# Kernel optimization log

Measured on AMD Instinct MI355X. Metric: run time of the kernel, lower is better.

The kernel has to match this reference:

```python
import math
import jax, jax.numpy as jnp
import numpy as np

L = 2          # num_layers
B = 2          # micro batch
S = 2048       # seq_length
H = 1024       # hidden_size
NH = 16        # num_attention_heads
DH = 64        # kv_channels (head dim)
FF = 4096      # ffn_hidden_size
EPS = 1e-5
STD = 0.0048


def setup_inputs() -> dict:
    key = jax.random.key(0)
    ks = jax.random.split(key, 12)
    out_std = STD / math.sqrt(2.0 * L)
    # ALiBi slopes for NH=16 (power of 2)
    start = 2.0 ** (-2.0 ** (-(math.log2(NH) - 3)))
    slopes = np.array([start * start ** i for i in range(NH)], dtype=np.float32)
    alibi = slopes[None, :, None, None] * np.arange(S, dtype=np.float32)[None, None, None, :]
    alibi = jnp.asarray(np.broadcast_to(alibi, (B, NH, 1, S)))  # [B, NH, 1, S]
    return {
        "hidden_states": jax.random.normal(ks[0], (B, S, H), jnp.float32),
        "alibi": alibi,
        "qkv_w": jax.random.normal(ks[1], (L, 3 * NH * DH, H), jnp.float32) * STD,
        "qkv_b": jnp.zeros((L, 3 * NH * DH), jnp.float32),
        "dense_w": jax.random.normal(ks[2], (L, H, NH * DH), jnp.float32) * out_std,
        "dense_b": jnp.zeros((L, H), jnp.float32),
        "mlp_w1": jax.random.normal(ks[3], (L, FF, H), jnp.float32) * STD,
        "mlp_b1": jnp.zeros((L, FF), jnp.float32),
        "mlp_w2": jax.random.normal(ks[4], (L, H, FF), jnp.float32) * out_std,
        "mlp_b2": jnp.zeros((L, H), jnp.float32),
        "ln1_w": jnp.ones((L, H), jnp.float32),
        "ln1_b": jnp.zeros((L, H), jnp.float32),
        "ln2_w": jnp.ones((L, H), jnp.float32),
        "ln2_b": jnp.zeros((L, H), jnp.float32),
    }


def _layernorm(x, w, b):
    mu = jnp.mean(x, axis=-1, keepdims=True)
    var = jnp.mean(jnp.square(x - mu), axis=-1, keepdims=True)
    return (x - mu) * jax.lax.rsqrt(var + EPS) * w + b


def _layer(x, alibi, causal, layer_number, qkv_w, qkv_b, dense_w, dense_b,
           mlp_w1, mlp_b1, mlp_w2, mlp_b2, ln1_w, ln1_b, ln2_w, ln2_b):
    # --- attention ---
    h = _layernorm(x, ln1_w, ln1_b)
    qkv = h @ qkv_w.T + qkv_b                       # [B, S, 3*NH*DH]
    q, k, v = jnp.split(qkv, 3, axis=-1)
    q = q.reshape(B, S, NH, DH).transpose(0, 2, 1, 3)  # [B, NH, S, DH]
    k = k.reshape(B, S, NH, DH).transpose(0, 2, 1, 3)
    v = v.reshape(B, S, NH, DH).transpose(0, 2, 1, 3)
    norm_factor = math.sqrt(DH) * layer_number
    beta = 1.0 / layer_number
    alpha = 1.0 / norm_factor
    scores = beta * alibi + alpha * jnp.einsum("bhqd,bhkd->bhqk", q, k)
    # ScaleMaskSoftmax: scale by layer_number, causal mask fill -10000, softmax
    scores = scores * layer_number
    scores = jnp.where(causal, scores, jnp.float32(-10000.0))
    probs = jax.nn.softmax(scores, axis=-1)
    ctx = jnp.einsum("bhqk,bhkd->bhqd", probs, v)   # [B, NH, S, DH]
    ctx = ctx.transpose(0, 2, 1, 3).reshape(B, S, NH * DH)
    attn_out = ctx @ dense_w.T + dense_b
    x = x + attn_out
    # --- MLP ---
    h2 = _layernorm(x, ln2_w, ln2_b)
    m = jax.nn.gelu(h2 @ mlp_w1.T + mlp_b1, approximate=False)
    m = m @ mlp_w2.T + mlp_b2
    return x + m


def reference(hidden_states, alibi, qkv_w, qkv_b, dense_w, dense_b,
              mlp_w1, mlp_b1, mlp_w2, mlp_b2, ln1_w, ln1_b, ln2_w, ln2_b):
    causal = jnp.tril(jnp.ones((S, S), dtype=bool))[None, None]  # [1,1,S,S]
    x = hidden_states
    for l in range(L):
        x = _layer(x, alibi, causal, l + 1,
                   qkv_w[l], qkv_b[l], dense_w[l], dense_b[l],
                   mlp_w1[l], mlp_b1[l], mlp_w2[l], mlp_b2[l],
                   ln1_w[l], ln1_b[l], ln2_w[l], ln2_b[l])
    return x
```

## Files before the change

### kernel.cpp

```cpp
#include <hip/hip_runtime.h>
#include <cstdint>
#include <cmath>

#define SS 2048
#define HH 1024

typedef __bf16 bf16_t;
typedef __bf16 bf16x8 __attribute__((ext_vector_type(8)));
typedef __bf16 bf16x4 __attribute__((ext_vector_type(4)));
typedef float  f32x4  __attribute__((ext_vector_type(4)));

union U32P { unsigned u; bf16_t h[2]; };

__device__ __forceinline__ void async_load16(const void* g, void* l) {
  __builtin_amdgcn_global_load_lds(
      (__attribute__((address_space(1))) void*)(g),
      (__attribute__((address_space(3))) void*)(l), 16, 0, 0);
}

__device__ __forceinline__ void bar_lds() {
  asm volatile("s_waitcnt lgkmcnt(0)" ::: "memory");
  __builtin_amdgcn_s_barrier();
}

__global__ __launch_bounds__(256) void cvt_kernel(const float* __restrict__ in,
                                                  bf16_t* __restrict__ out) {
  size_t i = (size_t)blockIdx.x * 256 + threadIdx.x;
  f32x4 v = ((const f32x4*)in)[i];
  bf16x4 o;
  o[0] = (bf16_t)v[0]; o[1] = (bf16_t)v[1]; o[2] = (bf16_t)v[2]; o[3] = (bf16_t)v[3];
  ((bf16x4*)out)[i] = o;
}

__global__ __launch_bounds__(256) void ln_kernel(const float* __restrict__ x,
                                                 const float* __restrict__ w,
                                                 const float* __restrict__ b,
                                                 bf16_t* __restrict__ out) {
  const int row = blockIdx.x;
  const int tid = threadIdx.x;
  const f32x4 v = ((const f32x4*)(x + (size_t)row * HH))[tid];
  float s  = v[0] + v[1] + v[2] + v[3];
  float s2 = v[0]*v[0] + v[1]*v[1] + v[2]*v[2] + v[3]*v[3];
#pragma unroll
  for (int o = 1; o < 64; o <<= 1) { s += __shfl_xor(s, o); s2 += __shfl_xor(s2, o); }
  __shared__ float r1[4], r2[4];
  if ((tid & 63) == 0) { r1[tid >> 6] = s; r2[tid >> 6] = s2; }
  __syncthreads();
  float ts  = r1[0] + r1[1] + r1[2] + r1[3];
  float ts2 = r2[0] + r2[1] + r2[2] + r2[3];
  float mu  = ts * (1.0f / HH);
  float var = ts2 * (1.0f / HH) - mu * mu;
  float rstd = rsqrtf(var + 1e-5f);
  f32x4 wv = ((const f32x4*)w)[tid];
  f32x4 bv = ((const f32x4*)b)[tid];
  bf16x4 o;
#pragma unroll
  for (int j = 0; j < 4; ++j) o[j] = (bf16_t)((v[j] - mu) * rstd * wv[j] + bv[j]);
  ((bf16x4*)(out + (size_t)row * HH))[tid] = o;
}

__device__ __forceinline__ float gelu_f(float x) {
  return 0.5f * x * (1.0f + erff(x * 0.70710678118654752f));
}

__global__ __launch_bounds__(256) void fuse_add(float* __restrict__ x,
                                                const bf16_t* __restrict__ p0,
                                                const bf16_t* __restrict__ p1,
                                                const float* __restrict__ bias) {
  size_t i = (size_t)blockIdx.x * 256 + threadIdx.x;
  f32x4 xv = ((f32x4*)x)[i];
  bf16x4 a = ((const bf16x4*)p0)[i];
  bf16x4 b4 = ((const bf16x4*)p1)[i];
  f32x4 bv = ((const f32x4*)bias)[i & 255];
#pragma unroll
  for (int j = 0; j < 4; ++j) xv[j] += (float)a[j] + (float)b4[j] + bv[j];
  ((f32x4*)x)[i] = xv;
}

template <int EPI>
__global__ __launch_bounds__(256) void gemm_bt(const bf16_t* __restrict__ A,
                                               const bf16_t* __restrict__ W,
                                               const float* __restrict__ bias,
                                               bf16_t* __restrict__ outb,
                                               int M, int N, int K) {
  __shared__ __align__(16) bf16_t As[128 * 64];
  __shared__ __align__(16) bf16_t Bs[128 * 64];
  const int tid = threadIdx.x;
  const int w = tid >> 6, lane = tid & 63;
  const int m16 = lane & 15, quad = lane >> 4;
  const int wm = w & 1, wn = w >> 1;
  const int n0 = blockIdx.x * 128, m0 = blockIdx.y * 128;

  f32x4 acc[4][4];
#pragma unroll
  for (int i = 0; i < 4; ++i)
#pragma unroll
    for (int j = 0; j < 4; ++j) acc[i][j] = (f32x4){0.f, 0.f, 0.f, 0.f};

  int rowi[4], gci[4];
#pragma unroll
  for (int i = 0; i < 4; ++i) {
    int p = (w * 4 + i) * 64 + lane;
    rowi[i] = p >> 3;
    gci[i] = ((lane & 7) ^ (rowi[i] & 7)) * 8;
  }

  for (int kt = 0; kt < K; kt += 64) {
    __syncthreads();
#pragma unroll
    for (int i = 0; i < 4; ++i) {
      async_load16(A + (size_t)(m0 + rowi[i]) * K + kt + gci[i], &As[(w * 4 + i) * 512]);
      async_load16(W + (size_t)(n0 + rowi[i]) * K + kt + gci[i], &Bs[(w * 4 + i) * 512]);
    }
    __syncthreads();
#pragma unroll
    for (int kk = 0; kk < 2; ++kk) {
      bf16x8 af[4], bfv[4];
#pragma unroll
      for (int mi = 0; mi < 4; ++mi) {
        int row = wm * 64 + mi * 16 + m16;
        int cpos = (kk * 4 + quad) ^ (row & 7);
        af[mi] = *(const bf16x8*)&As[row * 64 + cpos * 8];
      }
#pragma unroll
      for (int ni = 0; ni < 4; ++ni) {
        int row = wn * 64 + ni * 16 + m16;
        int cpos = (kk * 4 + quad) ^ (row & 7);
        bfv[ni] = *(const bf16x8*)&Bs[row * 64 + cpos * 8];
      }
#pragma unroll
      for (int mi = 0; mi < 4; ++mi)
#pragma unroll
        for (int ni = 0; ni < 4; ++ni)
          acc[mi][ni] = __builtin_amdgcn_mfma_f32_16x16x32_bf16(af[mi], bfv[ni],
                                                                acc[mi][ni], 0, 0, 0);
    }
  }

#pragma unroll
  for (int ni = 0; ni < 4; ++ni) {
    int col = n0 + wn * 64 + ni * 16 + m16;
    float bv = bias[col];
#pragma unroll
    for (int mi = 0; mi < 4; ++mi) {
      int rowb = m0 + wm * 64 + mi * 16 + quad * 4;
#pragma unroll
      for (int r = 0; r < 4; ++r) {
        size_t idx = (size_t)(rowb + r) * N + col;
        float v = acc[mi][ni][r] + bv;
        if constexpr (EPI == 1) v = gelu_f(v);
        outb[idx] = (bf16_t)v;
      }
    }
  }
}

__global__ __launch_bounds__(256) void gemm_qkv(const bf16_t* __restrict__ A,
                                                const bf16_t* __restrict__ W,
                                                const float* __restrict__ bias,
                                                bf16_t* __restrict__ qc,
                                                bf16_t* __restrict__ kc,
                                                bf16_t* __restrict__ vc) {
  const int M = 4096, N = 3072, K = 1024;
  __shared__ __align__(16) bf16_t As[128 * 64];
  __shared__ __align__(16) bf16_t Bs[128 * 64];
  const int tid = threadIdx.x;
  const int w = tid >> 6, lane = tid & 63;
  const int m16 = lane & 15, quad = lane >> 4;
  const int wm = w & 1, wn = w >> 1;
  const int n0 = blockIdx.x * 128, m0 = blockIdx.y * 128;

  f32x4 acc[4][4];
#pragma unroll
  for (int i = 0; i < 4; ++i)
#pragma unroll
    for (int j = 0; j < 4; ++j) acc[i][j] = (f32x4){0.f, 0.f, 0.f, 0.f};

  int rowi[4], gci[4];
#pragma unroll
  for (int i = 0; i < 4; ++i) {
    int p = (w * 4 + i) * 64 + lane;
    rowi[i] = p >> 3;
    gci[i] = ((lane & 7) ^ (rowi[i] & 7)) * 8;
  }

  for (int kt = 0; kt < K; kt += 64) {
    __syncthreads();
#pragma unroll
    for (int i = 0; i < 4; ++i) {
      async_load16(A + (size_t)(m0 + rowi[i]) * K + kt + gci[i], &As[(w * 4 + i) * 512]);
      async_load16(W + (size_t)(n0 + rowi[i]) * K + kt + gci[i], &Bs[(w * 4 + i) * 512]);
    }
    __syncthreads();
#pragma unroll
    for (int kk = 0; kk < 2; ++kk) {
      bf16x8 af[4], bfv[4];
#pragma unroll
      for (int mi = 0; mi < 4; ++mi) {
        int row = wm * 64 + mi * 16 + m16;
        int cpos = (kk * 4 + quad) ^ (row & 7);
        af[mi] = *(const bf16x8*)&As[row * 64 + cpos * 8];
      }
#pragma unroll
      for (int ni = 0; ni < 4; ++ni) {
        int row = wn * 64 + ni * 16 + m16;
        int cpos = (kk * 4 + quad) ^ (row & 7);
        bfv[ni] = *(const bf16x8*)&Bs[row * 64 + cpos * 8];
      }
#pragma unroll
      for (int mi = 0; mi < 4; ++mi)
#pragma unroll
        for (int ni = 0; ni < 4; ++ni)
          acc[mi][ni] = __builtin_amdgcn_mfma_f32_16x16x32_bf16(af[mi], bfv[ni],
                                                                acc[mi][ni], 0, 0, 0);
    }
  }

  const int bb = m0 >> 11;
  const int sbase = (m0 & 2047) + wm * 64;
#pragma unroll
  for (int ni = 0; ni < 4; ++ni) {
    int col = n0 + wn * 64 + ni * 16 + m16;
    float bv = bias[col];
    int region = col >> 10;
    int h = (col >> 6) & 15, d = col & 63;
#pragma unroll
    for (int mi = 0; mi < 4; ++mi) {
#pragma unroll
      for (int r = 0; r < 4; ++r) {
        int s = sbase + mi * 16 + quad * 4 + r;
        float v = acc[mi][ni][r] + bv;
        if (region == 0) {
          qc[(size_t)(bb * SS + s) * 1024 + col] = (bf16_t)v;
        } else {
          bf16_t* o = (region == 1) ? kc : vc;
          o[((size_t)(bb * 16 + h) * SS + s) * 64 + d] = (bf16_t)v;
        }
      }
    }
  }
}

__global__ __launch_bounds__(256) void gemm_sk2(const bf16_t* __restrict__ A,
                                                const bf16_t* __restrict__ W,
                                                bf16_t* __restrict__ p0,
                                                bf16_t* __restrict__ p1,
                                                int M, int N, int K) {
  __shared__ __align__(16) bf16_t As[128 * 64];
  __shared__ __align__(16) bf16_t Bs[128 * 64];
  const int tid = threadIdx.x;
  const int w = tid >> 6, lane = tid & 63;
  const int m16 = lane & 15, quad = lane >> 4;
  const int wm = w & 1, wn = w >> 1;
  const int n0 = blockIdx.x * 128, m0 = blockIdx.y * 128;
  const int z = blockIdx.z;
  const int kbeg = z * (K >> 1), kend = kbeg + (K >> 1);
  bf16_t* outb = z ? p1 : p0;

  f32x4 acc[4][4];
#pragma unroll
  for (int i = 0; i < 4; ++i)
#pragma unroll
    for (int j = 0; j < 4; ++j) acc[i][j] = (f32x4){0.f, 0.f, 0.f, 0.f};

  int rowi[4], gci[4];
#pragma unroll
  for (int i = 0; i < 4; ++i) {
    int p = (w * 4 + i) * 64 + lane;
    rowi[i] = p >> 3;
    gci[i] = ((lane & 7) ^ (rowi[i] & 7)) * 8;
  }

  for (int kt = kbeg; kt < kend; kt += 64) {
    __syncthreads();
#pragma unroll
    for (int i = 0; i < 4; ++i) {
      async_load16(A + (size_t)(m0 + rowi[i]) * K + kt + gci[i], &As[(w * 4 + i) * 512]);
      async_load16(W + (size_t)(n0 + rowi[i]) * K + kt + gci[i], &Bs[(w * 4 + i) * 512]);
    }
    __syncthreads();
#pragma unroll
    for (int kk = 0; kk < 2; ++kk) {
      bf16x8 af[4], bfv[4];
#pragma unroll
      for (int mi = 0; mi < 4; ++mi) {
        int row = wm * 64 + mi * 16 + m16;
        int cpos = (kk * 4 + quad) ^ (row & 7);
        af[mi] = *(const bf16x8*)&As[row * 64 + cpos * 8];
      }
#pragma unroll
      for (int ni = 0; ni < 4; ++ni) {
        int row = wn * 64 + ni * 16 + m16;
        int cpos = (kk * 4 + quad) ^ (row & 7);
        bfv[ni] = *(const bf16x8*)&Bs[row * 64 + cpos * 8];
      }
#pragma unroll
      for (int mi = 0; mi < 4; ++mi)
#pragma unroll
        for (int ni = 0; ni < 4; ++ni)
          acc[mi][ni] = __builtin_amdgcn_mfma_f32_16x16x32_bf16(af[mi], bfv[ni],
                                                                acc[mi][ni], 0, 0, 0);
    }
  }

#pragma unroll
  for (int ni = 0; ni < 4; ++ni) {
    int col = n0 + wn * 64 + ni * 16 + m16;
#pragma unroll
    for (int mi = 0; mi < 4; ++mi) {
      int rowb = m0 + wm * 64 + mi * 16 + quad * 4;
#pragma unroll
      for (int r = 0; r < 4; ++r) {
        size_t idx = (size_t)(rowb + r) * N + col;
        outb[idx] = (bf16_t)acc[mi][ni][r];
      }
    }
  }
}

__global__ __launch_bounds__(256) void attn_kernel(const bf16_t* __restrict__ qc,
                                                   const bf16_t* __restrict__ kc,
                                                   const bf16_t* __restrict__ vcp,
                                                   bf16_t* __restrict__ ctx,
                                                   bf16_t* __restrict__ pa0,
                                                   float* __restrict__ pl0,
                                                   bf16_t* __restrict__ pa1,
                                                   float* __restrict__ pl1) {
  const int qt = 31 - blockIdx.y;
  const int bh = blockIdx.x;
  const int b = bh >> 4, h = bh & 15;
  const int tid = threadIdx.x;
  const int w = tid >> 6, lane = tid & 63;
  const int m16 = lane & 15, quad = lane >> 4;

  const float slope2 = __builtin_amdgcn_exp2f(-0.70710678118654752f * (float)(h + 1))
                       * 1.4426950408889634f;
  const int wt = (int)((30.0f / slope2 + 63.0f) * 0.015625f);
  const int kt0 = (qt - wt > 0) ? (qt - wt) : 0;
  const int nch = (qt - kt0 + 8) >> 3;
  const int z = blockIdx.z;
  if (z >= nch) return;
  const int ktb = kt0 + z * 8;
  const int kte = (ktb + 7 < qt) ? (ktb + 7) : qt;
  const bool multi = (nch > 1);

  __shared__ __align__(16) bf16_t Vt[2][64 * 72];
  __shared__ __align__(16) bf16_t Pl[4][16 * 72];

  const int q_abs = qt * 64 + w * 16 + m16;
  float alkb[16];
#pragma unroll
  for (int kn = 0; kn < 4; ++kn)
#pragma unroll
    for (int r = 0; r < 4; ++r)
      alkb[kn * 4 + r] = slope2 * (float)(ktb * 64 + kn * 16 + quad * 4 + r - q_abs);
  const float d64 = slope2 * 64.0f;

  const int qrow = qt * 64 + w * 16 + m16;
  const bf16_t* qbase = qc + (size_t)(b * SS + qrow) * 1024 + h * 64;
  const bf16x8 bq0 = *(const bf16x8*)(qbase + quad * 8);
  const bf16x8 bq1 = *(const bf16x8*)(qbase + 32 + quad * 8);

  const bf16_t* kbase = kc + ((size_t)(b * 16 + h) * SS + m16) * 64 + quad * 8;
  const int kp2 = (tid & 31) * 2, vd0 = (tid >> 5) * 8;
  const bf16_t* vsrc = vcp + ((size_t)(b * 16 + h) * SS + kp2) * 64 + vd0;
  const int ql = w * 16 + m16;
  constexpr float C = 0.18033688011112042f;

  f32x4 acc[4];
#pragma unroll
  for (int i = 0; i < 4; ++i) acc[i] = (f32x4){0.f, 0.f, 0.f, 0.f};
  float rs_l = 0.f;

  bf16x8 ak[4][2], v0, v1;
  {
    const bf16_t* kb = kbase + (size_t)ktb * 4096;
#pragma unroll
    for (int kn = 0; kn < 4; ++kn) {
      ak[kn][0] = *(const bf16x8*)(kb + kn * 1024);
      ak[kn][1] = *(const bf16x8*)(kb + kn * 1024 + 32);
    }
    const bf16_t* vs = vsrc + (size_t)ktb * 4096;
    v0 = *(const bf16x8*)(vs);
    v1 = *(const bf16x8*)(vs + 64);
  }
#pragma unroll
  for (int j = 0; j < 8; ++j) {
    U32P pk; pk.h[0] = v0[j]; pk.h[1] = v1[j];
    *(unsigned*)&Vt[ktb & 1][(vd0 + j) * 72 + kp2] = pk.u;
  }

  for (int kt = ktb; kt <= kte; ++kt) {
    bar_lds();

    bf16x8 nk[4][2], nv0 = v0, nv1 = v1;
    if (kt < kte) {
      const bf16_t* kb = kbase + (size_t)(kt + 1) * 4096;
#pragma unroll
      for (int kn = 0; kn < 4; ++kn) {
        nk[kn][0] = *(const bf16x8*)(kb + kn * 1024);
        nk[kn][1] = *(const bf16x8*)(kb + kn * 1024 + 32);
      }
      const bf16_t* nsrc = vsrc + (size_t)(kt + 1) * 4096;
      nv0 = *(const bf16x8*)(nsrc);
      nv1 = *(const bf16x8*)(nsrc + 64);
    } else {
#pragma unroll
      for (int kn = 0; kn < 4; ++kn) { nk[kn][0] = ak[kn][0]; nk[kn][1] = ak[kn][1]; }
    }

    __builtin_amdgcn_s_setprio(1);
    float p[16];
    const bool diag = (kt == qt);
#pragma unroll
    for (int kn = 0; kn < 4; ++kn) {
      f32x4 zz = (f32x4){0.f, 0.f, 0.f, 0.f};
      zz = __builtin_amdgcn_mfma_f32_16x16x32_bf16(ak[kn][0], bq0, zz, 0, 0, 0);
      zz = __builtin_amdgcn_mfma_f32_16x16x32_bf16(ak[kn][1], bq1, zz, 0, 0, 0);
#pragma unroll
      for (int r = 0; r < 4; ++r) {
        float s = fmaf(zz[r], C, alkb[kn * 4 + r]);
        if (diag) {
          int kl = kn * 16 + quad * 4 + r;
          if (kl > ql) s = -INFINITY;
        }
        float e = __builtin_amdgcn_exp2f(s);
        p[kn * 4 + r] = e;
        rs_l += e;
      }
    }
#pragma unroll
    for (int i = 0; i < 16; ++i) alkb[i] += d64;

#pragma unroll
    for (int kn = 0; kn < 4; ++kn) {
      U32P a, c;
      a.h[0] = (bf16_t)p[kn * 4 + 0]; a.h[1] = (bf16_t)p[kn * 4 + 1];
      c.h[0] = (bf16_t)p[kn * 4 + 2]; c.h[1] = (bf16_t)p[kn * 4 + 3];
      uint2 pk; pk.x = a.u; pk.y = c.u;
      *(uint2*)&Pl[w][m16 * 72 + kn * 16 + quad * 4] = pk;
    }
    const bf16_t* vt = &Vt[kt & 1][0];
    bf16x8 bp0 = *(const bf16x8*)&Pl[w][m16 * 72 + quad * 8];
    bf16x8 bp1 = *(const bf16x8*)&Pl[w][m16 * 72 + 32 + quad * 8];
#pragma unroll
    for (int ni = 0; ni < 4; ++ni) {
      bf16x8 av0 = *(const bf16x8*)&vt[(ni * 16 + m16) * 72 + quad * 8];
      bf16x8 av1 = *(const bf16x8*)&vt[(ni * 16 + m16) * 72 + 32 + quad * 8];
      acc[ni] = __builtin_amdgcn_mfma_f32_16x16x32_bf16(av0, bp0, acc[ni], 0, 0, 0);
      acc[ni] = __builtin_amdgcn_mfma_f32_16x16x32_bf16(av1, bp1, acc[ni], 0, 0, 0);
    }
    __builtin_amdgcn_s_setprio(0);

    if (kt < kte) {
#pragma unroll
      for (int j = 0; j < 8; ++j) {
        U32P pk; pk.h[0] = nv0[j]; pk.h[1] = nv1[j];
        *(unsigned*)&Vt[(kt + 1) & 1][(vd0 + j) * 72 + kp2] = pk.u;
      }
    }
#pragma unroll
    for (int kn = 0; kn < 4; ++kn) { ak[kn][0] = nk[kn][0]; ak[kn][1] = nk[kn][1]; }
    v0 = nv0; v1 = nv1;
  }

  rs_l += __shfl_xor(rs_l, 16);
  rs_l += __shfl_xor(rs_l, 32);

  if (!multi) {
    const float inv_l = 1.0f / rs_l;
    bf16_t* cb = ctx + (size_t)(b * SS + qt * 64 + w * 16 + m16) * 1024 + h * 64;
#pragma unroll
    for (int ni = 0; ni < 4; ++ni) {
      U32P a, c;
      a.h[0] = (bf16_t)(acc[ni][0] * inv_l); a.h[1] = (bf16_t)(acc[ni][1] * inv_l);
      c.h[0] = (bf16_t)(acc[ni][2] * inv_l); c.h[1] = (bf16_t)(acc[ni][3] * inv_l);
      uint2 pk; pk.x = a.u; pk.y = c.u;
      *(uint2*)(cb + ni * 16 + quad * 4) = pk;
    }
  } else {
    const int sl = (h - 6) * 24 + (qt - 8);
    bf16_t* ab = (b ? pa1 : pa0) + (size_t)(sl * 4 + z) * 4096
                 + (size_t)(w * 16 + m16) * 64;
#pragma unroll
    for (int ni = 0; ni < 4; ++ni) {
      U32P a, c;
      a.h[0] = (bf16_t)acc[ni][0]; a.h[1] = (bf16_t)acc[ni][1];
      c.h[0] = (bf16_t)acc[ni][2]; c.h[1] = (bf16_t)acc[ni][3];
      uint2 pk; pk.x = a.u; pk.y = c.u;
      *(uint2*)(ab + ni * 16 + quad * 4) = pk;
    }
    if (quad == 0) (b ? pl1 : pl0)[(sl * 4 + z) * 64 + w * 16 + m16] = rs_l;
  }
}

__global__ __launch_bounds__(256) void attn_norm(const bf16_t* __restrict__ pa0,
                                                 const float* __restrict__ pl0,
                                                 const bf16_t* __restrict__ pa1,
                                                 const float* __restrict__ pl1,
                                                 bf16_t* __restrict__ ctx) {
  const int gs = blockIdx.x;
  const int b = gs >= 240, sl = b ? gs - 240 : gs;
  const int h = sl / 24 + 6, qt = sl % 24 + 8;
  const bf16_t* pa = b ? pa1 : pa0;
  const float* pl = b ? pl1 : pl0;
  const float slope2 = __builtin_amdgcn_exp2f(-0.70710678118654752f * (float)(h + 1))
                       * 1.4426950408889634f;
  const int wt = (int)((30.0f / slope2 + 63.0f) * 0.015625f);
  const int kt0 = (qt - wt > 0) ? (qt - wt) : 0;
  const int nch = (qt - kt0 + 8) >> 3;

  const int t = threadIdx.x;
  const int q = t >> 2, d0 = (t & 3) << 4;
  const bf16_t* ap = pa + (size_t)sl * 4 * 4096 + (size_t)q * 64 + d0;
  float av[16];
#pragma unroll
  for (int j = 0; j < 16; ++j) av[j] = 0.f;
  float l = 0.f;
  for (int z = 0; z < nch; ++z) {
    bf16x8 a0 = *(const bf16x8*)(ap + (size_t)z * 4096);
    bf16x8 a1 = *(const bf16x8*)(ap + (size_t)z * 4096 + 8);
#pragma unroll
    for (int j = 0; j < 8; ++j) { av[j] += (float)a0[j]; av[8 + j] += (float)a1[j]; }
    l += pl[(sl * 4 + z) * 64 + q];
  }
  const float invl = 1.0f / l;
  bf16_t* cp = ctx + (size_t)(b * SS + qt * 64 + q) * 1024 + h * 64 + d0;
  bf16x8 o0, o1;
#pragma unroll
  for (int j = 0; j < 8; ++j) o0[j] = (bf16_t)(av[j] * invl);
#pragma unroll
  for (int j = 0; j < 8; ++j) o1[j] = (bf16_t)(av[8 + j] * invl);
  *(bf16x8*)cp = o0;
  *(bf16x8*)(cp + 8) = o1;
}

extern "C" void kernel_launch(void* const* d_in, const int* in_sizes, int n_in,
                              void* d_out, int out_size, void* d_ws, size_t ws_size,
                              hipStream_t stream) {
  const float* hs    = (const float*)d_in[0];
  const float* qkvw  = (const float*)d_in[2];
  const float* qkvb  = (const float*)d_in[3];
  const float* dw    = (const float*)d_in[4];
  const float* db    = (const float*)d_in[5];
  const float* w1    = (const float*)d_in[6];
  const float* b1    = (const float*)d_in[7];
  const float* w2    = (const float*)d_in[8];
  const float* b2    = (const float*)d_in[9];
  const float* ln1w  = (const float*)d_in[10];
  const float* ln1b  = (const float*)d_in[11];
  const float* ln2w  = (const float*)d_in[12];
  const float* ln2b  = (const float*)d_in[13];
  float* x = (float*)d_out;

  char* ws = (char*)d_ws;
  bf16_t* wqc = (bf16_t*)(ws + 0);
  bf16_t* wdc = (bf16_t*)(ws + 12582912);
  bf16_t* w1c = (bf16_t*)(ws + 16777216);
  bf16_t* w2c = (bf16_t*)(ws + 33554432);
  bf16_t* hb  = (bf16_t*)(ws + 50331648);
  bf16_t* qm  = (bf16_t*)(ws + 58720256);
  bf16_t* cx  = (bf16_t*)(ws + 92274688);
  bf16_t* qc = (bf16_t*)(ws + 58720256);
  bf16_t* kc = (bf16_t*)(ws + 67108864);
  bf16_t* vc = (bf16_t*)(ws + 75497472);
  bf16_t* dp0 = qm;
  bf16_t* dp1 = qm + (size_t)4096 * 1024;
  bf16_t* pa0 = (bf16_t*)(ws + 50331648);
  float*  pl0 = (float*)(ws + 50331648 + (size_t)240 * 4 * 4096 * 2);
  bf16_t* pa1 = (bf16_t*)(ws + 83886080);
  float*  pl1 = (float*)(ws + 83886080 + (size_t)240 * 4 * 4096 * 2);

  hipMemcpyAsync(x, hs, (size_t)4096 * 1024 * 4, hipMemcpyDeviceToDevice, stream);
  cvt_kernel<<<6144, 256, 0, stream>>>(qkvw, wqc);
  cvt_kernel<<<2048, 256, 0, stream>>>(dw, wdc);
  cvt_kernel<<<8192, 256, 0, stream>>>(w1, w1c);
  cvt_kernel<<<8192, 256, 0, stream>>>(w2, w2c);

  for (int l = 0; l < 2; ++l) {
    ln_kernel<<<4096, 256, 0, stream>>>(x, ln1w + l * 1024, ln1b + l * 1024, hb);
    gemm_qkv<<<dim3(24, 32), 256, 0, stream>>>(hb, wqc + (size_t)l * 3145728,
        qkvb + l * 3072, qc, kc, vc);
    attn_kernel<<<dim3(32, 32, 4), 256, 0, stream>>>(qc, kc, vc, cx,
        pa0, pl0, pa1, pl1);
    attn_norm<<<480, 256, 0, stream>>>(pa0, pl0, pa1, pl1, cx);
    gemm_sk2<<<dim3(8, 32, 2), 256, 0, stream>>>(cx, wdc + (size_t)l * 1048576,
        dp0, dp1, 4096, 1024, 1024);
    fuse_add<<<4096, 256, 0, stream>>>(x, dp0, dp1, db + l * 1024);
    ln_kernel<<<4096, 256, 0, stream>>>(x, ln2w + l * 1024, ln2b + l * 1024, hb);
    gemm_bt<1><<<dim3(32, 32), 256, 0, stream>>>(hb, w1c + (size_t)l * 4194304,
        b1 + l * 4096, qm, 4096, 4096, 1024);
    gemm_sk2<<<dim3(8, 32, 2), 256, 0, stream>>>(qm, w2c + (size_t)l * 4194304,
        hb, cx, 4096, 1024, 4096);
    fuse_add<<<4096, 256, 0, stream>>>(x, hb, cx, b2 + l * 1024);
  }
}
```

Measured before the change: 744.5 us.

## Split attention blocks into single-wave workgroups without barriers or V double-buffering

The attention kernel now launches 64-thread single-wave blocks, with four times as many blocks along z, instead of 256-thread blocks of four waves. Each wave loads and transposes its own full V tile into private LDS and drops the shared double-buffered V tile, the s_barrier and the next-tile register prefetch. The aim is to remove cross-wave synchronisation stalls and give the scheduler finer-grained blocks to fill the GPU. In exchange, each K/V tile is read from memory four times as often and global loads no longer overlap with compute inside a block.

Result: slower. 807.9 us (+8.5%).

```diff
diff --git a/kernel.cpp b/kernel.cpp
--- a/kernel.cpp
+++ b/kernel.cpp
@@ -16,11 +16,6 @@
   __builtin_amdgcn_global_load_lds(
       (__attribute__((address_space(1))) void*)(g),
       (__attribute__((address_space(3))) void*)(l), 16, 0, 0);
-}
-
-__device__ __forceinline__ void bar_lds() {
-  asm volatile("s_waitcnt lgkmcnt(0)" ::: "memory");
-  __builtin_amdgcn_s_barrier();
 }
 
 __global__ __launch_bounds__(256) void cvt_kernel(const float* __restrict__ in,
@@ -161,7 +156,7 @@
                                                 bf16_t* __restrict__ qc,
                                                 bf16_t* __restrict__ kc,
                                                 bf16_t* __restrict__ vc) {
-  const int M = 4096, N = 3072, K = 1024;
+  const int K = 1024;
   __shared__ __align__(16) bf16_t As[128 * 64];
   __shared__ __align__(16) bf16_t Bs[128 * 64];
   const int tid = threadIdx.x;
@@ -318,36 +313,36 @@
   }
 }
 
-__global__ __launch_bounds__(256) void attn_kernel(const bf16_t* __restrict__ qc,
-                                                   const bf16_t* __restrict__ kc,
-                                                   const bf16_t* __restrict__ vcp,
-                                                   bf16_t* __restrict__ ctx,
-                                                   bf16_t* __restrict__ pa0,
-                                                   float* __restrict__ pl0,
-                                                   bf16_t* __restrict__ pa1,
-                                                   float* __restrict__ pl1) {
+__global__ __launch_bounds__(64) void attn_kernel(const bf16_t* __restrict__ qc,
+                                                  const bf16_t* __restrict__ kc,
+                                                  const bf16_t* __restrict__ vcp,
+                                                  bf16_t* __restrict__ ctx,
+                                                  bf16_t* __restrict__ pa0,
+                                                  float* __restrict__ pl0,
+                                                  bf16_t* __restrict__ pa1,
+                                                  float* __restrict__ pl1) {
   const int qt = 31 - blockIdx.y;
   const int bh = blockIdx.x;
   const int b = bh >> 4, h = bh & 15;
+  const int sl4 = blockIdx.z & 3;
   const int tid = threadIdx.x;
-  const int w = tid >> 6, lane = tid & 63;
-  const int m16 = lane & 15, quad = lane >> 4;
+  const int m16 = tid & 15, quad = tid >> 4;
 
   const float slope2 = __builtin_amdgcn_exp2f(-0.70710678118654752f * (float)(h + 1))
                        * 1.4426950408889634f;
   const int wt = (int)((30.0f / slope2 + 63.0f) * 0.015625f);
   const int kt0 = (qt - wt > 0) ? (qt - wt) : 0;
   const int nch = (qt - kt0 + 8) >> 3;
-  const int z = blockIdx.z;
+  const int z = blockIdx.z >> 2;
   if (z >= nch) return;
   const int ktb = kt0 + z * 8;
   const int kte = (ktb + 7 < qt) ? (ktb + 7) : qt;
   const bool multi = (nch > 1);
 
-  __shared__ __align__(16) bf16_t Vt[2][64 * 72];
-  __shared__ __align__(16) bf16_t Pl[4][16 * 72];
-
-  const int q_abs = qt * 64 + w * 16 + m16;
+  __shared__ __align__(16) bf16_t Vt[64 * 72];
+  __shared__ __align__(16) bf16_t Pl[16 * 72];
+
+  const int q_abs = qt * 64 + sl4 * 16 + m16;
   float alkb[16];
 #pragma unroll
   for (int kn = 0; kn < 4; ++kn)
@@ -356,15 +351,14 @@
       alkb[kn * 4 + r] = slope2 * (float)(ktb * 64 + kn * 16 + quad * 4 + r - q_abs);
   const float d64 = slope2 * 64.0f;
 
-  const int qrow = qt * 64 + w * 16 + m16;
-  const bf16_t* qbase = qc + (size_t)(b * SS + qrow) * 1024 + h * 64;
+  const bf16_t* qbase = qc + (size_t)(b * SS + q_abs) * 1024 + h * 64;
   const bf16x8 bq0 = *(const bf16x8*)(qbase + quad * 8);
   const bf16x8 bq1 = *(const bf16x8*)(qbase + 32 + quad * 8);
 
   const bf16_t* kbase = kc + ((size_t)(b * 16 + h) * SS + m16) * 64 + quad * 8;
-  const int kp2 = (tid & 31) * 2, vd0 = (tid >> 5) * 8;
-  const bf16_t* vsrc = vcp + ((size_t)(b * 16 + h) * SS + kp2) * 64 + vd0;
-  const int ql = w * 16 + m16;
+  const int k0 = (tid & 31) * 2, dblk = (tid >> 5) * 32;
+  const bf16_t* vsrc = vcp + ((size_t)(b * 16 + h) * SS + k0) * 64 + dblk;
+  const int ql = sl4 * 16 + m16;
   constexpr float C = 0.18033688011112042f;
 
   f32x4 acc[4];
@@ -372,51 +366,30 @@
   for (int i = 0; i < 4; ++i) acc[i] = (f32x4){0.f, 0.f, 0.f, 0.f};
   float rs_l = 0.f;
 
-  bf16x8 ak[4][2], v0, v1;
-  {
-    const bf16_t* kb = kbase + (size_t)ktb * 4096;
+  for (int kt = ktb; kt <= kte; ++kt) {
+    const bf16_t* kb = kbase + (size_t)kt * 4096;
+    bf16x8 kf[4][2];
 #pragma unroll
     for (int kn = 0; kn < 4; ++kn) {
-      ak[kn][0] = *(const bf16x8*)(kb + kn * 1024);
-      ak[kn][1] = *(const bf16x8*)(kb + kn * 1024 + 32);
-    }
-    const bf16_t* vs = vsrc + (size_t)ktb * 4096;
-    v0 = *(const bf16x8*)(vs);
-    v1 = *(const bf16x8*)(vs + 64);
-  }
-#pragma unroll
-  for (int j = 0; j < 8; ++j) {
-    U32P pk; pk.h[0] = v0[j]; pk.h[1] = v1[j];
-    *(unsigned*)&Vt[ktb & 1][(vd0 + j) * 72 + kp2] = pk.u;
-  }
-
-  for (int kt = ktb; kt <= kte; ++kt) {
-    bar_lds();
-
-    bf16x8 nk[4][2], nv0 = v0, nv1 = v1;
-    if (kt < kte) {
-      const bf16_t* kb = kbase + (size_t)(kt + 1) * 4096;
-#pragma unroll
-      for (int kn = 0; kn < 4; ++kn) {
-        nk[kn][0] = *(const bf16x8*)(kb + kn * 1024);
-        nk[kn][1] = *(const bf16x8*)(kb + kn * 1024 + 32);
-      }
-      const bf16_t* nsrc = vsrc + (size_t)(kt + 1) * 4096;
-      nv0 = *(const bf16x8*)(nsrc);
-      nv1 = *(const bf16x8*)(nsrc + 64);
-    } else {
-#pragma unroll
-      for (int kn = 0; kn < 4; ++kn) { nk[kn][0] = ak[kn][0]; nk[kn][1] = ak[kn][1]; }
+      kf[kn][0] = *(const bf16x8*)(kb + kn * 1024);
+      kf[kn][1] = *(const bf16x8*)(kb + kn * 1024 + 32);
+    }
+    const bf16_t* vs = vsrc + (size_t)kt * 4096;
+    bf16x8 va0[4], va1[4];
+#pragma unroll
+    for (int c = 0; c < 4; ++c) {
+      va0[c] = *(const bf16x8*)(vs + c * 8);
+      va1[c] = *(const bf16x8*)(vs + 64 + c * 8);
     }
 
     __builtin_amdgcn_s_setprio(1);
-    float p[16];
     const bool diag = (kt == qt);
 #pragma unroll
     for (int kn = 0; kn < 4; ++kn) {
       f32x4 zz = (f32x4){0.f, 0.f, 0.f, 0.f};
-      zz = __builtin_amdgcn_mfma_f32_16x16x32_bf16(ak[kn][0], bq0, zz, 0, 0, 0);
-      zz = __builtin_amdgcn_mfma_f32_16x16x32_bf16(ak[kn][1], bq1, zz, 0, 0, 0);
+      zz = __builtin_amdgcn_mfma_f32_16x16x32_bf16(kf[kn][0], bq0, zz, 0, 0, 0);
+      zz = __builtin_amdgcn_mfma_f32_16x16x32_bf16(kf[kn][1], bq1, zz, 0, 0, 0);
+      f32x4 ev;
 #pragma unroll
       for (int r = 0; r < 4; ++r) {
         float s = fmaf(zz[r], C, alkb[kn * 4 + r]);
@@ -424,44 +397,36 @@
           int kl = kn * 16 + quad * 4 + r;
           if (kl > ql) s = -INFINITY;
         }
-        float e = __builtin_amdgcn_exp2f(s);
-        p[kn * 4 + r] = e;
-        rs_l += e;
-      }
+        ev[r] = __builtin_amdgcn_exp2f(s);
+        rs_l += ev[r];
+      }
+      U32P a, c;
+      a.h[0] = (bf16_t)ev[0]; a.h[1] = (bf16_t)ev[1];
+      c.h[0] = (bf16_t)ev[2]; c.h[1] = (bf16_t)ev[3];
+      uint2 pk; pk.x = a.u; pk.y = c.u;
+      *(uint2*)&Pl[m16 * 72 + kn * 16 + quad * 4] = pk;
     }
 #pragma unroll
     for (int i = 0; i < 16; ++i) alkb[i] += d64;
 
 #pragma unroll
-    for (int kn = 0; kn < 4; ++kn) {
-      U32P a, c;
-      a.h[0] = (bf16_t)p[kn * 4 + 0]; a.h[1] = (bf16_t)p[kn * 4 + 1];
-      c.h[0] = (bf16_t)p[kn * 4 + 2]; c.h[1] = (bf16_t)p[kn * 4 + 3];
-      uint2 pk; pk.x = a.u; pk.y = c.u;
-      *(uint2*)&Pl[w][m16 * 72 + kn * 16 + quad * 4] = pk;
-    }
-    const bf16_t* vt = &Vt[kt & 1][0];
-    bf16x8 bp0 = *(const bf16x8*)&Pl[w][m16 * 72 + quad * 8];
-    bf16x8 bp1 = *(const bf16x8*)&Pl[w][m16 * 72 + 32 + quad * 8];
+    for (int c = 0; c < 4; ++c)
+#pragma unroll
+      for (int j = 0; j < 8; ++j) {
+        U32P pk; pk.h[0] = va0[c][j]; pk.h[1] = va1[c][j];
+        *(unsigned*)&Vt[(dblk + c * 8 + j) * 72 + k0] = pk.u;
+      }
+
+    bf16x8 bp0 = *(const bf16x8*)&Pl[m16 * 72 + quad * 8];
+    bf16x8 bp1 = *(const bf16x8*)&Pl[m16 * 72 + 32 + quad * 8];
 #pragma unroll
     for (int ni = 0; ni < 4; ++ni) {
-      bf16x8 av0 = *(const bf16x8*)&vt[(ni * 16 + m16) * 72 + quad * 8];
-      bf16x8 av1 = *(const bf16x8*)&vt[(ni * 16 + m16) * 72 + 32 + quad * 8];
+      bf16x8 av0 = *(const bf16x8*)&Vt[(ni * 16 + m16) * 72 + quad * 8];
+      bf16x8 av1 = *(const bf16x8*)&Vt[(ni * 16 + m16) * 72 + 32 + quad * 8];
       acc[ni] = __builtin_amdgcn_mfma_f32_16x16x32_bf16(av0, bp0, acc[ni], 0, 0, 0);
       acc[ni] = __builtin_amdgcn_mfma_f32_16x16x32_bf16(av1, bp1, acc[ni], 0, 0, 0);
     }
     __builtin_amdgcn_s_setprio(0);
-
-    if (kt < kte) {
-#pragma unroll
-      for (int j = 0; j < 8; ++j) {
-        U32P pk; pk.h[0] = nv0[j]; pk.h[1] = nv1[j];
-        *(unsigned*)&Vt[(kt + 1) & 1][(vd0 + j) * 72 + kp2] = pk.u;
-      }
-    }
-#pragma unroll
-    for (int kn = 0; kn < 4; ++kn) { ak[kn][0] = nk[kn][0]; ak[kn][1] = nk[kn][1]; }
-    v0 = nv0; v1 = nv1;
   }
 
   rs_l += __shfl_xor(rs_l, 16);
@@ -469,7 +434,7 @@
 
   if (!multi) {
     const float inv_l = 1.0f / rs_l;
-    bf16_t* cb = ctx + (size_t)(b * SS + qt * 64 + w * 16 + m16) * 1024 + h * 64;
+    bf16_t* cb = ctx + (size_t)(b * SS + q_abs) * 1024 + h * 64;
 #pragma unroll
     for (int ni = 0; ni < 4; ++ni) {
       U32P a, c;
@@ -481,7 +446,7 @@
   } else {
     const int sl = (h - 6) * 24 + (qt - 8);
     bf16_t* ab = (b ? pa1 : pa0) + (size_t)(sl * 4 + z) * 4096
-                 + (size_t)(w * 16 + m16) * 64;
+                 + (size_t)(sl4 * 16 + m16) * 64;
 #pragma unroll
     for (int ni = 0; ni < 4; ++ni) {
       U32P a, c;
@@ -490,7 +455,7 @@
       uint2 pk; pk.x = a.u; pk.y = c.u;
       *(uint2*)(ab + ni * 16 + quad * 4) = pk;
     }
-    if (quad == 0) (b ? pl1 : pl0)[(sl * 4 + z) * 64 + w * 16 + m16] = rs_l;
+    if (quad == 0) (b ? pl1 : pl0)[(sl * 4 + z) * 64 + sl4 * 16 + m16] = rs_l;
   }
 }
 
@@ -581,7 +546,7 @@
     ln_kernel<<<4096, 256, 0, stream>>>(x, ln1w + l * 1024, ln1b + l * 1024, hb);
     gemm_qkv<<<dim3(24, 32), 256, 0, stream>>>(hb, wqc + (size_t)l * 3145728,
         qkvb + l * 3072, qc, kc, vc);
-    attn_kernel<<<dim3(32, 32, 4), 256, 0, stream>>>(qc, kc, vc, cx,
+    attn_kernel<<<dim3(32, 32, 16), 64, 0, stream>>>(qc, kc, vc, cx,
         pa0, pl0, pa1, pl1);
     attn_norm<<<480, 256, 0, stream>>>(pa0, pl0, pa1, pl1, cx);
     gemm_sk2<<<dim3(8, 32, 2), 256, 0, stream>>>(cx, wdc + (size_t)l * 1048576,
```
